# Kernel tuning notes

Measured on AMD Instinct MI355X. Metric: run time of the kernel, lower is better.

Reference implementation:

```python
import jax, jax.numpy as jnp
import numpy as np
from jax import lax

B_, L_ = 4, 512
D_MODEL, N_LAYER = 384, 4
D_INNER, N_STATE, DT_RANK, D_CONV = 768, 16, 24, 4
VOCAB, FEAT = 1544, 1536


def setup_inputs() -> dict:
    key = jax.random.key(0)
    ks = iter(jax.random.split(key, 32))
    nrm = lambda shape, s=0.02: jax.random.normal(next(ks), shape, jnp.float32) * s
    input_ids = jax.random.normal(next(ks), (B_, L_, VOCAB), jnp.float32)
    return dict(
        input_ids=input_ids,
        fc_W=nrm((D_MODEL, VOCAB)), fc_b=jnp.zeros((D_MODEL,), jnp.float32),
        in_proj_W=nrm((N_LAYER, 2 * D_INNER, D_MODEL)),
        conv_W=nrm((N_LAYER, D_INNER, 1, D_CONV), 0.2),
        conv_b=jnp.zeros((N_LAYER, D_INNER), jnp.float32),
        x_proj_W=nrm((N_LAYER, DT_RANK + 2 * N_STATE, D_INNER)),
        dt_proj_W=nrm((N_LAYER, D_INNER, DT_RANK)),
        dt_proj_b=jnp.zeros((N_LAYER, D_INNER), jnp.float32),
        A_log=jnp.tile(jnp.log(jnp.arange(1, N_STATE + 1, dtype=jnp.float32)), (N_LAYER, D_INNER, 1)),
        D=jnp.ones((N_LAYER, D_INNER), jnp.float32),
        out_proj_W=nrm((N_LAYER, D_MODEL, D_INNER)),
        norm_W=jnp.ones((N_LAYER, D_MODEL), jnp.float32),
        normf_W=jnp.ones((D_MODEL,), jnp.float32),
        head_W=nrm((FEAT, D_MODEL)),
    )


def _rmsnorm(x, w, eps=1e-5):
    return x * lax.rsqrt(jnp.mean(x * x, axis=-1, keepdims=True) + eps) * w


def _selective_scan(u, delta, A, B, C, D):
    # u, delta: (b, l, d); A: (d, n); B, C: (b, l, n); D: (d,)
    dA = jnp.exp(jnp.einsum('bld,dn->bldn', delta, A))          # (b, l, d, n)
    dBu = jnp.einsum('bld,bln->bldn', delta * u, B)             # (b, l, d, n)
    b, l, d = u.shape
    n = A.shape[1]

    def step(h, inp):
        dA_t, dBu_t, c_t = inp                                   # (b,d,n),(b,d,n),(b,n)
        h = dA_t * h + dBu_t
        y = jnp.einsum('bdn,bn->bd', h, c_t)
        return h, y

    h0 = jnp.zeros((b, d, n), u.dtype)
    _, ys = lax.scan(step, h0, (dA.transpose(1, 0, 2, 3), dBu.transpose(1, 0, 2, 3), C.transpose(1, 0, 2)))
    return ys.transpose(1, 0, 2) + u * D                         # (b, l, d)


def _mamba(input_ids, fc_W, fc_b, in_proj_W, conv_W, conv_b, x_proj_W,
           dt_proj_W, dt_proj_b, A_log, D, out_proj_W, norm_W, normf_W, head_W):
    x = input_ids @ fc_W.T + fc_b                                # (b, l, d_model)
    for i in range(N_LAYER):
        h = _rmsnorm(x, norm_W[i])
        xz = h @ in_proj_W[i].T                                  # (b, l, 2*d_inner)
        xc, res = jnp.split(xz, 2, axis=-1)
        xc = xc.transpose(0, 2, 1)                               # (b, d_inner, l)
        xc = lax.conv_general_dilated(
            xc, conv_W[i], window_strides=(1,), padding=[(D_CONV - 1, 0)],
            feature_group_count=D_INNER, dimension_numbers=('NCH', 'OIH', 'NCH'))
        xc = xc + conv_b[i][None, :, None]
        u = jax.nn.silu(xc.transpose(0, 2, 1))                   # (b, l, d_inner)
        x_dbl = u @ x_proj_W[i].T
        delta, Bm, Cm = jnp.split(x_dbl, [DT_RANK, DT_RANK + N_STATE], axis=-1)
        delta = jax.nn.softplus(delta @ dt_proj_W[i].T + dt_proj_b[i])
        A = -jnp.exp(A_log[i])
        y = _selective_scan(u, delta, A, Bm, Cm, D[i])
        y = y * jax.nn.silu(res)
        x = y @ out_proj_W[i].T + x                              # residual
    x = _rmsnorm(x, normf_W)
    return x @ head_W.T                                          # (b, l, feat)


def reference(input_ids, fc_W, fc_b, in_proj_W, conv_W, conv_b, x_proj_W,
              dt_proj_W, dt_proj_b, A_log, D, out_proj_W, norm_W, normf_W, head_W):
    return _mamba(input_ids, fc_W, fc_b, in_proj_W, conv_W, conv_b, x_proj_W,
                  dt_proj_W, dt_proj_b, A_log, D, out_proj_W, norm_W, normf_W, head_W)
```

## Files before the change

### kernel.cpp

```cpp
#include <hip/hip_runtime.h>
#include <math.h>

#define B_ 4
#define L_ 512
#define MROWS 2048
#define D_MODEL 384
#define N_LAYER 4
#define D_INNER 768
#define N_STATE 16
#define DT_RANK 24
#define D_CONV 4
#define VOCAB 1544
#define FEAT 1536
#define XPROJ_N 56
#define NCH 16
#define SCH 32
#define DG 2

typedef __attribute__((ext_vector_type(8))) short short8;
typedef __attribute__((ext_vector_type(4))) float floatx4;

__device__ __forceinline__ float softplus_f(float x) { return x > 20.f ? x : log1pf(expf(x)); }
__device__ __forceinline__ float silu_f(float x) { return x / (1.f + __expf(-x)); }

__device__ __forceinline__ unsigned pack2bf(float x, float y) {
    unsigned ux = __float_as_uint(x); ux = (ux + 0x7FFFu + ((ux >> 16) & 1u)) >> 16;
    unsigned uy = __float_as_uint(y); uy = (uy + 0x7FFFu + ((uy >> 16) & 1u)) >> 16;
    return ux | (uy << 16);
}

template <int CTRL>
__device__ __forceinline__ float dpp_radd(float x) {
    int r = __builtin_amdgcn_update_dpp(0, __float_as_int(x), CTRL, 0xf, 0xf, true);
    return x + __int_as_float(r);
}

__device__ __forceinline__ void wave_lds_fence() {
    asm volatile("s_waitcnt lgkmcnt(0)" ::: "memory");
    __builtin_amdgcn_wave_barrier();
}

__device__ __forceinline__ float4 ld4_guard(const float* __restrict__ p, int k, int ke) {
    if (k + 3 < ke) return *(const float4*)(p + k);
    float4 r = make_float4(0.f, 0.f, 0.f, 0.f);
    if (k + 0 < ke) r.x = p[k + 0];
    if (k + 1 < ke) r.y = p[k + 1];
    if (k + 2 < ke) r.z = p[k + 2];
    return r;
}

__device__ __forceinline__ short8 ld8h_guard(const short* __restrict__ p, int k, int ke) {
    if (k + 7 < ke) return *(const short8*)(p + k);
    short8 r = {0, 0, 0, 0, 0, 0, 0, 0};
#pragma unroll
    for (int j = 0; j < 8; ++j)
        if (k + j < ke) r[j] = p[k + j];
    return r;
}

struct CastDesc {
    const float* src[6];
    short*       dst[6];
    unsigned     cum[6];
};

__global__ __launch_bounds__(256) void cast_w_k(CastDesc cd, unsigned total4,
                                                float4* __restrict__ zb, unsigned z4)
{
    unsigned i = blockIdx.x * 256 + threadIdx.x;
    if (i < total4) {
        int s = 0;
#pragma unroll
        for (int j = 0; j < 5; ++j)
            if (i >= cd.cum[j] && s == j) s = j + 1;
        unsigned off = i - (s ? cd.cum[s - 1] : 0u);
        float4 v = ((const float4*)cd.src[s])[off];
        uint2 pk;
        pk.x = pack2bf(v.x, v.y);
        pk.y = pack2bf(v.z, v.w);
        ((uint2*)cd.dst[s])[off] = pk;
    } else {
        unsigned zi = i - total4;
        if (zi < z4) zb[zi] = make_float4(0.f, 0.f, 0.f, 0.f);
    }
}

#define ASTR 40

template <int EPI, bool GATED, bool ATOMIC, bool RMSN, bool NG, bool ABF>
__global__ __launch_bounds__(256) void mfma_gemm(
    const float* __restrict__ A, const short* __restrict__ Abf,
    const short* __restrict__ Wb,
    const float* __restrict__ bias, const float* __restrict__ gate,
    const float* __restrict__ nw,
    float* __restrict__ C, int M, int N, int K, int lda, int ldg, int ldc, int KC)
{
    __shared__ short As[2][64 * ASTR];
    __shared__ short Ws[2][64 * ASTR];
    __shared__ float sscale[64];

    const int t  = threadIdx.x;
    const int m0 = blockIdx.y * 64;
    const int n0 = blockIdx.x * 64;
    const int ks = blockIdx.z * KC;
    const int ke = min(K, ks + KC);

    const int srow = t >> 2;
    const int sseg = (t & 3) * 8;

    if (RMSN) {
        const int row = t >> 2, q = t & 3;
        const float* xr = A + (size_t)(m0 + row) * lda + q * (K >> 2);
        float s = 0.f;
        for (int i = 0; i < (K >> 2); i += 4) {
            float4 v = *(const float4*)(xr + i);
            s += v.x * v.x + v.y * v.y + v.z * v.z + v.w * v.w;
        }
        s += __shfl_xor(s, 1, 64);
        s += __shfl_xor(s, 2, 64);
        if (q == 0) sscale[row] = rsqrtf(s / (float)K + 1e-5f);
        __syncthreads();
    }

    float4 ra0, ra1, rg0, rg1, rn0, rn1;
    short8 ra8, rw8;

    auto prefetch = [&](int k0) {
        if (ABF) {
            ra8 = ld8h_guard(Abf + (size_t)(m0 + srow) * lda, k0 + sseg, ke);
        } else {
            const float* ar = A + (size_t)(m0 + srow) * lda;
            ra0 = ld4_guard(ar, k0 + sseg, ke);
            ra1 = ld4_guard(ar, k0 + sseg + 4, ke);
            if (GATED) {
                const float* gr = gate + (size_t)(m0 + srow) * ldg;
                rg0 = ld4_guard(gr, k0 + sseg, ke);
                rg1 = ld4_guard(gr, k0 + sseg + 4, ke);
            }
            if (RMSN) {
                rn0 = ld4_guard(nw, k0 + sseg, ke);
                rn1 = ld4_guard(nw, k0 + sseg + 4, ke);
            }
        }
        if (!NG || (n0 + srow) < N) {
            rw8 = ld8h_guard(Wb + (size_t)(n0 + srow) * (size_t)K, k0 + sseg, ke);
        } else {
            rw8 = (short8){0, 0, 0, 0, 0, 0, 0, 0};
        }
    };

    auto stage = [&](int p) {
        if (ABF) {
            *(short8*)&As[p][srow * ASTR + sseg] = ra8;
        } else {
            float4 a0 = ra0, a1 = ra1;
            if (GATED) {
                a0.x *= silu_f(rg0.x); a0.y *= silu_f(rg0.y); a0.z *= silu_f(rg0.z); a0.w *= silu_f(rg0.w);
                a1.x *= silu_f(rg1.x); a1.y *= silu_f(rg1.y); a1.z *= silu_f(rg1.z); a1.w *= silu_f(rg1.w);
            }
            if (RMSN) {
                float sc = sscale[srow];
                a0.x *= sc * rn0.x; a0.y *= sc * rn0.y; a0.z *= sc * rn0.z; a0.w *= sc * rn0.w;
                a1.x *= sc * rn1.x; a1.y *= sc * rn1.y; a1.z *= sc * rn1.z; a1.w *= sc * rn1.w;
            }
            int4 pa;
            pa.x = pack2bf(a0.x, a0.y); pa.y = pack2bf(a0.z, a0.w);
            pa.z = pack2bf(a1.x, a1.y); pa.w = pack2bf(a1.z, a1.w);
            *(int4*)&As[p][srow * ASTR + sseg] = pa;
        }
        *(short8*)&Ws[p][srow * ASTR + sseg] = rw8;
    };

    prefetch(ks);
    stage(0);
    if (ks + 32 < ke) prefetch(ks + 32);
    __syncthreads();

    floatx4 acc[2][2];
#pragma unroll
    for (int i = 0; i < 2; ++i)
#pragma unroll
        for (int j = 0; j < 2; ++j) acc[i][j] = (floatx4){0.f, 0.f, 0.f, 0.f};

    const int w    = t >> 6;
    const int lane = t & 63;
    const int quad = lane >> 4;
    const int lm   = lane & 15;
    const int aoff = ((w >> 1) * 32 + lm) * ASTR + quad * 8;
    const int boff = ((w & 1) * 32 + lm) * ASTR + quad * 8;

    int p = 0;
    for (int k0 = ks; k0 < ke; k0 += 32) {
        const bool more = (k0 + 32 < ke);
        if (more) {
            stage(p ^ 1);
            if (k0 + 64 < ke) prefetch(k0 + 64);
        }
        short8 a0 = *(const short8*)&As[p][aoff];
        short8 a1 = *(const short8*)&As[p][aoff + 16 * ASTR];
        short8 b0 = *(const short8*)&Ws[p][boff];
        short8 b1 = *(const short8*)&Ws[p][boff + 16 * ASTR];
        acc[0][0] = __builtin_amdgcn_mfma_f32_16x16x32_bf16(a0, b0, acc[0][0], 0, 0, 0);
        acc[0][1] = __builtin_amdgcn_mfma_f32_16x16x32_bf16(a0, b1, acc[0][1], 0, 0, 0);
        acc[1][0] = __builtin_amdgcn_mfma_f32_16x16x32_bf16(a1, b0, acc[1][0], 0, 0, 0);
        acc[1][1] = __builtin_amdgcn_mfma_f32_16x16x32_bf16(a1, b1, acc[1][1], 0, 0, 0);
        if (more) {
            __syncthreads();
            p ^= 1;
        }
    }

    const int rbase = m0 + (w >> 1) * 32 + quad * 4;
    const int cbase = n0 + (w & 1) * 32 + lm;
#pragma unroll
    for (int mt = 0; mt < 2; ++mt)
#pragma unroll
        for (int nt = 0; nt < 2; ++nt) {
            const int gc = cbase + nt * 16;
            if (NG && gc >= N) continue;
#pragma unroll
            for (int r = 0; r < 4; ++r) {
                const size_t gr = rbase + mt * 16 + r;
                float v = acc[mt][nt][r];
                if (ATOMIC) {
                    if (EPI == 1 && blockIdx.z == 0) v += bias[gc];
                    atomicAdd(&C[gr * ldc + gc], v);
                } else {
                    if (EPI == 1) v += bias[gc];
                    if (EPI == 2) v = softplus_f(v + bias[gc]);
                    C[gr * ldc + gc] = v;
                }
            }
        }
}

__global__ __launch_bounds__(256) void conv_silu_k(
    const float* __restrict__ xz, const float* __restrict__ w,
    const float* __restrict__ cb, float* __restrict__ u, short* __restrict__ ubf)
{
    int idx = blockIdx.x * 256 + threadIdx.x;
    if (idx >= MROWS * (D_INNER / 4)) return;
    int dq = idx % (D_INNER / 4);
    int m  = idx / (D_INNER / 4);
    int d0 = dq * 4;
    int b = m / L_, l = m % L_;
    float4 wq[4];
#pragma unroll
    for (int j = 0; j < 4; ++j) wq[j] = *(const float4*)(w + (d0 + j) * D_CONV);
    float acc[4];
#pragma unroll
    for (int j = 0; j < 4; ++j) acc[j] = cb[d0 + j];
#pragma unroll
    for (int tt = 0; tt < 4; ++tt) {
        int ll = l - 3 + tt;
        if (ll >= 0) {
            float4 xv = *(const float4*)(xz + (size_t)(b * L_ + ll) * (2 * D_INNER) + d0);
            acc[0] = fmaf(xv.x, ((const float*)&wq[0])[tt], acc[0]);
            acc[1] = fmaf(xv.y, ((const float*)&wq[1])[tt], acc[1]);
            acc[2] = fmaf(xv.z, ((const float*)&wq[2])[tt], acc[2]);
            acc[3] = fmaf(xv.w, ((const float*)&wq[3])[tt], acc[3]);
        }
    }
    float4 o = make_float4(silu_f(acc[0]), silu_f(acc[1]), silu_f(acc[2]), silu_f(acc[3]));
    *(float4*)(u + (size_t)m * D_INNER + d0) = o;
    uint2 pk;
    pk.x = pack2bf(o.x, o.y);
    pk.y = pack2bf(o.z, o.w);
    *(uint2*)(ubf + (size_t)m * D_INNER + d0) = pk;
}

__global__ __launch_bounds__(512, 4) void scan_fused_k(
    const float* __restrict__ xdbl, const float* __restrict__ u,
    const float* __restrict__ xz,
    const float* __restrict__ dtW, const float* __restrict__ dtb,
    const float* __restrict__ A_log, const float* __restrict__ Dp,
    short* __restrict__ ybf)
{
    __shared__ __align__(16) float sd[NCH][SCH][DG];
    __shared__ __align__(16) float su[NCH][SCH][DG];
    __shared__ __align__(16) float sy[NCH][SCH][DG];
    __shared__ float sP[NCH][DG][16], sH[NCH][DG][16];

    const int t  = threadIdx.x;
    const int w  = t >> 6;
    const int l  = t & 63;
    const int ch = l >> 5;
    const int c  = w * 2 + ch;
    const int dl = (l >> 4) & 1;
    const int n  = l & 15;
    const int bx  = blockIdx.x;
    const int dgi = (bx & 7) * (D_INNER / DG / 8) + (bx >> 3);
    const int d0 = dgi * DG;
    const int d  = d0 + dl;
    const int b  = blockIdx.y;

    const int tc = t >> 5, tj = t & 31;
    const size_t trow = (size_t)b * L_ + t;

    float2 rv  = *(const float2*)(xz + trow * (2 * D_INNER) + D_INNER + d0);
    float2 uv2 = *(const float2*)(u + trow * D_INNER + d0);
    *(float2*)&su[tc][tj][0] = uv2;

    {
        float4 w4[6];
#pragma unroll
        for (int q = 0; q < 6; ++q) w4[q] = *(const float4*)(dtW + (size_t)d * DT_RANK + q * 4);
        const float bias = dtb[d];
#pragma unroll
        for (int rr = 0; rr < 2; ++rr) {
            const int j = n * 2 + rr;
            const float* xr = xdbl + ((size_t)b * L_ + c * SCH + j) * XPROJ_N;
            float acc = bias;
#pragma unroll
            for (int q = 0; q < 6; ++q) {
                float4 xv = *(const float4*)(xr + q * 4);
                acc = fmaf(xv.x, w4[q].x, acc);
                acc = fmaf(xv.y, w4[q].y, acc);
                acc = fmaf(xv.z, w4[q].z, acc);
                acc = fmaf(xv.w, w4[q].w, acc);
            }
            sd[c][j][dl] = softplus_f(acc);
        }
    }
    wave_lds_fence();

    const float Av = -expf(A_log[d * N_STATE + n]);
    const float Dd = Dp[d];
    const float* xbn = xdbl + ((size_t)b * L_ + c * SCH) * XPROJ_N + DT_RANK + n;

    {
        float h = 0.f, sdv = 0.f;
        float rB[8];
#pragma unroll
        for (int q = 0; q < 8; ++q) rB[q] = xbn[q * XPROJ_N];
#pragma unroll
        for (int g = 0; g < SCH / 8; ++g) {
            float nB[8];
            if (g + 1 < SCH / 8) {
#pragma unroll
                for (int q = 0; q < 8; ++q) nB[q] = xbn[(g * 8 + 8 + q) * XPROJ_N];
            }
#pragma unroll
            for (int q = 0; q < 8; ++q) {
                const int j = g * 8 + q;
                float dv = sd[c][j][dl];
                float uv = su[c][j][dl];
                float e  = __expf(dv * Av);
                h = fmaf(e, h, dv * uv * rB[q]);
                sdv += dv;
            }
#pragma unroll
            for (int q = 0; q < 8; ++q) rB[q] = nB[q];
        }
        sP[c][dl][n] = __expf(sdv * Av);
        sH[c][dl][n] = h;
    }

    float rB[8], rC[8];
#pragma unroll
    for (int q = 0; q < 8; ++q) {
        rB[q] = xbn[q * XPROJ_N];
        rC[q] = xbn[q * XPROJ_N + N_STATE];
    }
    __syncthreads();

    float hs = 0.f;
    for (int s = 0; s < c; ++s)
        hs = fmaf(sP[s][dl][n], hs, sH[s][dl][n]);

    {
        float h = hs;
#pragma unroll
        for (int g = 0; g < SCH / 8; ++g) {
            float nB[8], nC[8];
            if (g + 1 < SCH / 8) {
#pragma unroll
                for (int q = 0; q < 8; ++q) {
                    nB[q] = xbn[(g * 8 + 8 + q) * XPROJ_N];
                    nC[q] = xbn[(g * 8 + 8 + q) * XPROJ_N + N_STATE];
                }
            }
#pragma unroll
            for (int q = 0; q < 8; ++q) {
                const int j = g * 8 + q;
                float dv = sd[c][j][dl];
                float uv = su[c][j][dl];
                float e  = __expf(dv * Av);
                h = fmaf(e, h, dv * uv * rB[q]);
                float p = h * rC[q];
                p = dpp_radd<0x128>(p);
                p = dpp_radd<0x124>(p);
                p = dpp_radd<0x122>(p);
                p = dpp_radd<0x121>(p);
                if (n == 0) sy[c][j][dl] = fmaf(uv, Dd, p);
            }
#pragma unroll
            for (int q = 0; q < 8; ++q) { rB[q] = nB[q]; rC[q] = nC[q]; }
        }
    }
    wave_lds_fence();

    {
        float2 yv = *(const float2*)&sy[tc][tj][0];
        float o0 = yv.x * silu_f(rv.x);
        float o1 = yv.y * silu_f(rv.y);
        *(unsigned*)(ybf + trow * D_INNER + d0) = pack2bf(o0, o1);
    }
}

extern "C" void kernel_launch(void* const* d_in, const int* in_sizes, int n_in,
                              void* d_out, int out_size, void* d_ws, size_t ws_size,
                              hipStream_t stream)
{
    const float* input_ids = (const float*)d_in[0];
    const float* fc_W      = (const float*)d_in[1];
    const float* fc_b      = (const float*)d_in[2];
    const float* in_proj_W = (const float*)d_in[3];
    const float* conv_W    = (const float*)d_in[4];
    const float* conv_b    = (const float*)d_in[5];
    const float* x_proj_W  = (const float*)d_in[6];
    const float* dt_proj_W = (const float*)d_in[7];
    const float* dt_proj_b = (const float*)d_in[8];
    const float* A_log     = (const float*)d_in[9];
    const float* Dp        = (const float*)d_in[10];
    const float* out_proj_W= (const float*)d_in[11];
    const float* norm_W    = (const float*)d_in[12];
    const float* normf_W   = (const float*)d_in[13];
    const float* head_W    = (const float*)d_in[14];
    float* out = (float*)d_out;

    float* ws       = (float*)d_ws;
    float* x_ws     = ws;
    float* xdbl_ws  = x_ws    + (size_t)MROWS * D_MODEL;
    float* xz_ws    = xdbl_ws + (size_t)N_LAYER * MROWS * XPROJ_N;
    float* u_ws     = xz_ws   + (size_t)MROWS * 2 * D_INNER;
    short* bf       = (short*)(u_ws + (size_t)MROWS * D_INNER);
    short* wbf_fc   = bf;
    short* wbf_in   = wbf_fc  + (size_t)D_MODEL * VOCAB;
    short* wbf_x    = wbf_in  + (size_t)N_LAYER * 2 * D_INNER * D_MODEL;
    short* wbf_out  = wbf_x   + (size_t)N_LAYER * XPROJ_N * D_INNER;
    short* wbf_head = wbf_out + (size_t)N_LAYER * D_MODEL * D_INNER;
    short* ids_bf   = wbf_head+ (size_t)FEAT * D_MODEL;
    short* ubf_ws   = ids_bf  + (size_t)MROWS * VOCAB;
    short* ybf_ws   = ubf_ws  + (size_t)MROWS * D_INNER;

    const dim3 blk(256);
    const dim3 blk512(512);

    CastDesc cd;
    cd.src[0] = fc_W;       cd.dst[0] = wbf_fc;
    cd.src[1] = in_proj_W;  cd.dst[1] = wbf_in;
    cd.src[2] = x_proj_W;   cd.dst[2] = wbf_x;
    cd.src[3] = out_proj_W; cd.dst[3] = wbf_out;
    cd.src[4] = head_W;     cd.dst[4] = wbf_head;
    cd.src[5] = input_ids;  cd.dst[5] = ids_bf;
    unsigned c0 = (unsigned)(D_MODEL * VOCAB / 4);
    unsigned c1 = c0 + (unsigned)(N_LAYER * 2 * D_INNER * D_MODEL / 4);
    unsigned c2 = c1 + (unsigned)(N_LAYER * XPROJ_N * D_INNER / 4);
    unsigned c3 = c2 + (unsigned)(N_LAYER * D_INNER * DT_RANK / 4 * 0 + N_LAYER * D_MODEL * D_INNER / 4);
    unsigned c4 = c3 + (unsigned)(FEAT * D_MODEL / 4);
    unsigned c5 = c4 + (unsigned)(MROWS * VOCAB / 4);
    cd.cum[0] = c0; cd.cum[1] = c1; cd.cum[2] = c2;
    cd.cum[3] = c3; cd.cum[4] = c4; cd.cum[5] = c5;
    const unsigned zero4 = (unsigned)((MROWS * D_MODEL + N_LAYER * MROWS * XPROJ_N) / 4);
    cast_w_k<<<(c5 + zero4 + 255) / 256, blk, 0, stream>>>(cd, c5, (float4*)x_ws, zero4);

    mfma_gemm<1, false, true, false, false, true><<<dim3(D_MODEL / 64, MROWS / 64, 7), blk, 0, stream>>>(
        nullptr, ids_bf, wbf_fc, fc_b, nullptr, nullptr, x_ws,
        MROWS, D_MODEL, VOCAB, VOCAB, 0, D_MODEL, 256);

    for (int i = 0; i < N_LAYER; ++i) {
        float* xdbl_i = xdbl_ws + (size_t)i * MROWS * XPROJ_N;

        mfma_gemm<0, false, false, true, false, false><<<dim3(2 * D_INNER / 64, MROWS / 64, 1), blk, 0, stream>>>(
            x_ws, nullptr, wbf_in + (size_t)i * 2 * D_INNER * D_MODEL,
            nullptr, nullptr, norm_W + i * D_MODEL, xz_ws,
            MROWS, 2 * D_INNER, D_MODEL, D_MODEL, 0, 2 * D_INNER, D_MODEL);

        conv_silu_k<<<(MROWS * (D_INNER / 4) + 255) / 256, blk, 0, stream>>>(
            xz_ws, conv_W + (size_t)i * D_INNER * D_CONV, conv_b + i * D_INNER,
            u_ws, ubf_ws);

        mfma_gemm<0, false, true, false, true, true><<<dim3(1, MROWS / 64, 6), blk, 0, stream>>>(
            nullptr, ubf_ws, wbf_x + (size_t)i * XPROJ_N * D_INNER,
            nullptr, nullptr, nullptr, xdbl_i,
            MROWS, XPROJ_N, D_INNER, D_INNER, 0, XPROJ_N, 128);

        scan_fused_k<<<dim3(D_INNER / DG, B_), blk512, 0, stream>>>(
            xdbl_i, u_ws, xz_ws,
            dt_proj_W + (size_t)i * D_INNER * DT_RANK, dt_proj_b + i * D_INNER,
            A_log + (size_t)i * D_INNER * N_STATE, Dp + i * D_INNER, ybf_ws);

        mfma_gemm<0, false, true, false, false, true><<<dim3(D_MODEL / 64, MROWS / 64, 2), blk, 0, stream>>>(
            nullptr, ybf_ws, wbf_out + (size_t)i * D_MODEL * D_INNER,
            nullptr, nullptr, nullptr, x_ws,
            MROWS, D_MODEL, D_INNER, D_INNER, 0, D_MODEL, 384);
    }

    mfma_gemm<0, false, false, true, false, false><<<dim3(FEAT / 64, MROWS / 64, 1), blk, 0, stream>>>(
        x_ws, nullptr, wbf_head, nullptr, nullptr, normf_W, out,
        MROWS, FEAT, D_MODEL, D_MODEL, 0, FEAT, D_MODEL);
}
```

Baseline: 521.2 us.

## Split RMSNorm into a bf16 cast kernel and restructure scan LDS layout

Moves RMSNorm out of the GEMM prologue into a standalone kernel that writes normalized bf16 activations, so the in_proj and head GEMMs read bf16 A tiles directly instead of recomputing row norms and converting fp32 in every block. The scan kernel now computes the dt projection once per timestep row for both channels, packs delta and u into one float2 LDS array, packs the chunk prefix P/H into one array, and unrolls the cross-chunk combine with a mask. This adds five kernel launches and an extra bf16 buffer round trip, in exchange for less redundant norm work and fewer scattered LDS accesses.

```diff
diff --git a/kernel.cpp b/kernel.cpp
--- a/kernel.cpp
+++ b/kernel.cpp
@@ -85,19 +85,44 @@
     }
 }
 
+__global__ __launch_bounds__(256) void rmsnorm_cast_k(
+    const float* __restrict__ x, const float* __restrict__ nw,
+    unsigned* __restrict__ outp)
+{
+    const int idx = blockIdx.x * 256 + threadIdx.x;
+    const int row = idx >> 3, q = idx & 7;
+    const float* xr = x + (size_t)row * D_MODEL + q * 48;
+    float4 v[12];
+    float s = 0.f;
+#pragma unroll
+    for (int i = 0; i < 12; ++i) {
+        v[i] = *(const float4*)(xr + i * 4);
+        s += v[i].x * v[i].x + v[i].y * v[i].y + v[i].z * v[i].z + v[i].w * v[i].w;
+    }
+    s += __shfl_xor(s, 1, 64);
+    s += __shfl_xor(s, 2, 64);
+    s += __shfl_xor(s, 4, 64);
+    const float sc = rsqrtf(s / (float)D_MODEL + 1e-5f);
+    unsigned* op = outp + ((size_t)row * D_MODEL + q * 48) / 2;
+#pragma unroll
+    for (int i = 0; i < 12; ++i) {
+        float4 wv = *(const float4*)(nw + q * 48 + i * 4);
+        op[i * 2]     = pack2bf(v[i].x * (sc * wv.x), v[i].y * (sc * wv.y));
+        op[i * 2 + 1] = pack2bf(v[i].z * (sc * wv.z), v[i].w * (sc * wv.w));
+    }
+}
+
 #define ASTR 40
 
-template <int EPI, bool GATED, bool ATOMIC, bool RMSN, bool NG, bool ABF>
+template <int EPI, bool ATOMIC, bool NG, bool ABF>
 __global__ __launch_bounds__(256) void mfma_gemm(
     const float* __restrict__ A, const short* __restrict__ Abf,
     const short* __restrict__ Wb,
-    const float* __restrict__ bias, const float* __restrict__ gate,
-    const float* __restrict__ nw,
-    float* __restrict__ C, int M, int N, int K, int lda, int ldg, int ldc, int KC)
+    const float* __restrict__ bias,
+    float* __restrict__ C, int M, int N, int K, int lda, int ldc, int KC)
 {
     __shared__ short As[2][64 * ASTR];
     __shared__ short Ws[2][64 * ASTR];
-    __shared__ float sscale[64];
 
     const int t  = threadIdx.x;
     const int m0 = blockIdx.y * 64;
@@ -108,21 +133,7 @@
     const int srow = t >> 2;
     const int sseg = (t & 3) * 8;
 
-    if (RMSN) {
-        const int row = t >> 2, q = t & 3;
-        const float* xr = A + (size_t)(m0 + row) * lda + q * (K >> 2);
-        float s = 0.f;
-        for (int i = 0; i < (K >> 2); i += 4) {
-            float4 v = *(const float4*)(xr + i);
-            s += v.x * v.x + v.y * v.y + v.z * v.z + v.w * v.w;
-        }
-        s += __shfl_xor(s, 1, 64);
-        s += __shfl_xor(s, 2, 64);
-        if (q == 0) sscale[row] = rsqrtf(s / (float)K + 1e-5f);
-        __syncthreads();
-    }
-
-    float4 ra0, ra1, rg0, rg1, rn0, rn1;
+    float4 ra0, ra1;
     short8 ra8, rw8;
 
     auto prefetch = [&](int k0) {
@@ -132,15 +143,6 @@
             const float* ar = A + (size_t)(m0 + srow) * lda;
             ra0 = ld4_guard(ar, k0 + sseg, ke);
             ra1 = ld4_guard(ar, k0 + sseg + 4, ke);
-            if (GATED) {
-                const float* gr = gate + (size_t)(m0 + srow) * ldg;
-                rg0 = ld4_guard(gr, k0 + sseg, ke);
-                rg1 = ld4_guard(gr, k0 + sseg + 4, ke);
-            }
-            if (RMSN) {
-                rn0 = ld4_guard(nw, k0 + sseg, ke);
-                rn1 = ld4_guard(nw, k0 + sseg + 4, ke);
-            }
         }
         if (!NG || (n0 + srow) < N) {
             rw8 = ld8h_guard(Wb + (size_t)(n0 + srow) * (size_t)K, k0 + sseg, ke);
@@ -153,19 +155,9 @@
         if (ABF) {
             *(short8*)&As[p][srow * ASTR + sseg] = ra8;
         } else {
-            float4 a0 = ra0, a1 = ra1;
-            if (GATED) {
-                a0.x *= silu_f(rg0.x); a0.y *= silu_f(rg0.y); a0.z *= silu_f(rg0.z); a0.w *= silu_f(rg0.w);
-                a1.x *= silu_f(rg1.x); a1.y *= silu_f(rg1.y); a1.z *= silu_f(rg1.z); a1.w *= silu_f(rg1.w);
-            }
-            if (RMSN) {
-                float sc = sscale[srow];
-                a0.x *= sc * rn0.x; a0.y *= sc * rn0.y; a0.z *= sc * rn0.z; a0.w *= sc * rn0.w;
-                a1.x *= sc * rn1.x; a1.y *= sc * rn1.y; a1.z *= sc * rn1.z; a1.w *= sc * rn1.w;
-            }
             int4 pa;
-            pa.x = pack2bf(a0.x, a0.y); pa.y = pack2bf(a0.z, a0.w);
-            pa.z = pack2bf(a1.x, a1.y); pa.w = pack2bf(a1.z, a1.w);
+            pa.x = pack2bf(ra0.x, ra0.y); pa.y = pack2bf(ra0.z, ra0.w);
+            pa.z = pack2bf(ra1.x, ra1.y); pa.w = pack2bf(ra1.z, ra1.w);
             *(int4*)&As[p][srow * ASTR + sseg] = pa;
         }
         *(short8*)&Ws[p][srow * ASTR + sseg] = rw8;
@@ -276,10 +268,9 @@
     const float* __restrict__ A_log, const float* __restrict__ Dp,
     short* __restrict__ ybf)
 {
-    __shared__ __align__(16) float sd[NCH][SCH][DG];
-    __shared__ __align__(16) float su[NCH][SCH][DG];
-    __shared__ __align__(16) float sy[NCH][SCH][DG];
-    __shared__ float sP[NCH][DG][16], sH[NCH][DG][16];
+    __shared__ __align__(16) float2 sdu[NCH][SCH][DG];
+    __shared__ __align__(16) float  sy[NCH][SCH][DG];
+    __shared__ __align__(16) float2 sPH[NCH][DG][16];
 
     const int t  = threadIdx.x;
     const int w  = t >> 6;
@@ -299,28 +290,24 @@
 
     float2 rv  = *(const float2*)(xz + trow * (2 * D_INNER) + D_INNER + d0);
     float2 uv2 = *(const float2*)(u + trow * D_INNER + d0);
-    *(float2*)&su[tc][tj][0] = uv2;
 
     {
-        float4 w4[6];
-#pragma unroll
-        for (int q = 0; q < 6; ++q) w4[q] = *(const float4*)(dtW + (size_t)d * DT_RANK + q * 4);
-        const float bias = dtb[d];
-#pragma unroll
-        for (int rr = 0; rr < 2; ++rr) {
-            const int j = n * 2 + rr;
-            const float* xr = xdbl + ((size_t)b * L_ + c * SCH + j) * XPROJ_N;
-            float acc = bias;
-#pragma unroll
-            for (int q = 0; q < 6; ++q) {
-                float4 xv = *(const float4*)(xr + q * 4);
-                acc = fmaf(xv.x, w4[q].x, acc);
-                acc = fmaf(xv.y, w4[q].y, acc);
-                acc = fmaf(xv.z, w4[q].z, acc);
-                acc = fmaf(xv.w, w4[q].w, acc);
-            }
-            sd[c][j][dl] = softplus_f(acc);
-        }
+        const float* wd = dtW + (size_t)d0 * DT_RANK;
+        const float* xr = xdbl + trow * XPROJ_N;
+        float acc0 = dtb[d0];
+        float acc1 = dtb[d0 + 1];
+#pragma unroll
+        for (int q = 0; q < 6; ++q) {
+            float4 xv = *(const float4*)(xr + q * 4);
+            float4 w0 = *(const float4*)(wd + q * 4);
+            float4 w1 = *(const float4*)(wd + DT_RANK + q * 4);
+            acc0 = fmaf(xv.x, w0.x, acc0); acc0 = fmaf(xv.y, w0.y, acc0);
+            acc0 = fmaf(xv.z, w0.z, acc0); acc0 = fmaf(xv.w, w0.w, acc0);
+            acc1 = fmaf(xv.x, w1.x, acc1); acc1 = fmaf(xv.y, w1.y, acc1);
+            acc1 = fmaf(xv.z, w1.z, acc1); acc1 = fmaf(xv.w, w1.w, acc1);
+        }
+        float4 pk = make_float4(softplus_f(acc0), uv2.x, softplus_f(acc1), uv2.y);
+        *(float4*)&sdu[tc][tj][0] = pk;
     }
     wave_lds_fence();
 
@@ -343,17 +330,18 @@
 #pragma unroll
             for (int q = 0; q < 8; ++q) {
                 const int j = g * 8 + q;
-                float dv = sd[c][j][dl];
-                float uv = su[c][j][dl];
-                float e  = __expf(dv * Av);
-                h = fmaf(e, h, dv * uv * rB[q]);
-                sdv += dv;
+                float2 du = *(const float2*)&sdu[c][j][dl];
+                float e  = __expf(du.x * Av);
+                h = fmaf(e, h, du.x * du.y * rB[q]);
+                sdv += du.x;
             }
 #pragma unroll
             for (int q = 0; q < 8; ++q) rB[q] = nB[q];
         }
-        sP[c][dl][n] = __expf(sdv * Av);
-        sH[c][dl][n] = h;
+        float2 ph;
+        ph.x = __expf(sdv * Av);
+        ph.y = h;
+        *(float2*)&sPH[c][dl][n] = ph;
     }
 
     float rB[8], rC[8];
@@ -365,8 +353,12 @@
     __syncthreads();
 
     float hs = 0.f;
-    for (int s = 0; s < c; ++s)
-        hs = fmaf(sP[s][dl][n], hs, sH[s][dl][n]);
+#pragma unroll
+    for (int s = 0; s < NCH - 1; ++s) {
+        float2 ph = *(const float2*)&sPH[s][dl][n];
+        const bool m = s < c;
+        hs = fmaf(m ? ph.x : 1.f, hs, m ? ph.y : 0.f);
+    }
 
     {
         float h = hs;
@@ -383,16 +375,15 @@
 #pragma unroll
             for (int q = 0; q < 8; ++q) {
                 const int j = g * 8 + q;
-                float dv = sd[c][j][dl];
-                float uv = su[c][j][dl];
-                float e  = __expf(dv * Av);
-                h = fmaf(e, h, dv * uv * rB[q]);
+                float2 du = *(const float2*)&sdu[c][j][dl];
+                float e  = __expf(du.x * Av);
+                h = fmaf(e, h, du.x * du.y * rB[q]);
                 float p = h * rC[q];
                 p = dpp_radd<0x128>(p);
                 p = dpp_radd<0x124>(p);
                 p = dpp_radd<0x122>(p);
                 p = dpp_radd<0x121>(p);
-                if (n == 0) sy[c][j][dl] = fmaf(uv, Dd, p);
+                if (n == 0) sy[c][j][dl] = fmaf(du.y, Dd, p);
             }
 #pragma unroll
             for (int q = 0; q < 8; ++q) { rB[q] = nB[q]; rC[q] = nC[q]; }
@@ -443,6 +434,7 @@
     short* ids_bf   = wbf_head+ (size_t)FEAT * D_MODEL;
     short* ubf_ws   = ids_bf  + (size_t)MROWS * VOCAB;
     short* ybf_ws   = ubf_ws  + (size_t)MROWS * D_INNER;
+    short* xnorm_bf = ybf_ws  + (size_t)MROWS * D_INNER;
 
     const dim3 blk(256);
     const dim3 blk512(512);
@@ -457,7 +449,7 @@
     unsigned c0 = (unsigned)(D_MODEL * VOCAB / 4);
     unsigned c1 = c0 + (unsigned)(N_LAYER * 2 * D_INNER * D_MODEL / 4);
     unsigned c2 = c1 + (unsigned)(N_LAYER * XPROJ_N * D_INNER / 4);
-    unsigned c3 = c2 + (unsigned)(N_LAYER * D_INNER * DT_RANK / 4 * 0 + N_LAYER * D_MODEL * D_INNER / 4);
+    unsigned c3 = c2 + (unsigned)(N_LAYER * D_MODEL * D_INNER / 4);
     unsigned c4 = c3 + (unsigned)(FEAT * D_MODEL / 4);
     unsigned c5 = c4 + (unsigned)(MROWS * VOCAB / 4);
     cd.cum[0] = c0; cd.cum[1] = c1; cd.cum[2] = c2;
@@ -465,39 +457,44 @@
     const unsigned zero4 = (unsigned)((MROWS * D_MODEL + N_LAYER * MROWS * XPROJ_N) / 4);
     cast_w_k<<<(c5 + zero4 + 255) / 256, blk, 0, stream>>>(cd, c5, (float4*)x_ws, zero4);
 
-    mfma_gemm<1, false, true, false, false, true><<<dim3(D_MODEL / 64, MROWS / 64, 7), blk, 0, stream>>>(
-        nullptr, ids_bf, wbf_fc, fc_b, nullptr, nullptr, x_ws,
-        MROWS, D_MODEL, VOCAB, VOCAB, 0, D_MODEL, 256);
+    mfma_gemm<1, true, false, true><<<dim3(D_MODEL / 64, MROWS / 64, 7), blk, 0, stream>>>(
+        nullptr, ids_bf, wbf_fc, fc_b, x_ws,
+        MROWS, D_MODEL, VOCAB, VOCAB, D_MODEL, 256);
 
     for (int i = 0; i < N_LAYER; ++i) {
         float* xdbl_i = xdbl_ws + (size_t)i * MROWS * XPROJ_N;
 
-        mfma_gemm<0, false, false, true, false, false><<<dim3(2 * D_INNER / 64, MROWS / 64, 1), blk, 0, stream>>>(
-            x_ws, nullptr, wbf_in + (size_t)i * 2 * D_INNER * D_MODEL,
-            nullptr, nullptr, norm_W + i * D_MODEL, xz_ws,
-            MROWS, 2 * D_INNER, D_MODEL, D_MODEL, 0, 2 * D_INNER, D_MODEL);
+        rmsnorm_cast_k<<<MROWS * 8 / 256, blk, 0, stream>>>(
+            x_ws, norm_W + i * D_MODEL, (unsigned*)xnorm_bf);
+
+        mfma_gemm<0, false, false, true><<<dim3(2 * D_INNER / 64, MROWS / 64, 1), blk, 0, stream>>>(
+            nullptr, xnorm_bf, wbf_in + (size_t)i * 2 * D_INNER * D_MODEL,
+            nullptr, xz_ws,
+            MROWS, 2 * D_INNER, D_MODEL, D_MODEL, 2 * D_INNER, D_MODEL);
 
         conv_silu_k<<<(MROWS * (D_INNER / 4) + 255) / 256, blk, 0, stream>>>(
             xz_ws, conv_W + (size_t)i * D_INNER * D_CONV, conv_b + i * D_INNER,
             u_ws, ubf_ws);
 
-        mfma_gemm<0, false, true, false, true, true><<<dim3(1, MROWS / 64, 6), blk, 0, stream>>>(
+        mfma_gemm<0, true, true, true><<<dim3(1, MROWS / 64, 6), blk, 0, stream>>>(
             nullptr, ubf_ws, wbf_x + (size_t)i * XPROJ_N * D_INNER,
-            nullptr, nullptr, nullptr, xdbl_i,
-            MROWS, XPROJ_N, D_INNER, D_INNER, 0, XPROJ_N, 128);
+            nullptr, xdbl_i,
+            MROWS, XPROJ_N, D_INNER, D_INNER, XPROJ_N, 128);
 
         scan_fused_k<<<dim3(D_INNER / DG, B_), blk512, 0, stream>>>(
             xdbl_i, u_ws, xz_ws,
             dt_proj_W + (size_t)i * D_INNER * DT_RANK, dt_proj_b + i * D_INNER,
             A_log + (size_t)i * D_INNER * N_STATE, Dp + i * D_INNER, ybf_ws);
 
-        mfma_gemm<0, false, true, false, false, true><<<dim3(D_MODEL / 64, MROWS / 64, 2), blk, 0, stream>>>(
+        mfma_gemm<0, true, false, true><<<dim3(D_MODEL / 64, MROWS / 64, 2), blk, 0, stream>>>(
             nullptr, ybf_ws, wbf_out + (size_t)i * D_MODEL * D_INNER,
-            nullptr, nullptr, nullptr, x_ws,
-            MROWS, D_MODEL, D_INNER, D_INNER, 0, D_MODEL, 384);
-    }
-
-    mfma_gemm<0, false, false, true, false, false><<<dim3(FEAT / 64, MROWS / 64, 1), blk, 0, stream>>>(
-        x_ws, nullptr, wbf_head, nullptr, nullptr, normf_W, out,
-        MROWS, FEAT, D_MODEL, D_MODEL, 0, FEAT, D_MODEL);
-}
+            nullptr, x_ws,
+            MROWS, D_MODEL, D_INNER, D_INNER, D_MODEL, 384);
+    }
+
+    rmsnorm_cast_k<<<MROWS * 8 / 256, blk, 0, stream>>>(
+        x_ws, normf_W, (unsigned*)xnorm_bf);
+    mfma_gemm<0, false, false, true><<<dim3(FEAT / 64, MROWS / 64, 1), blk, 0, stream>>>(
+        nullptr, xnorm_bf, wbf_head, nullptr, out,
+        MROWS, FEAT, D_MODEL, D_MODEL, FEAT, D_MODEL);
+}
```

Result: faster. 428.5 us (-17.8%).
